# Performance work log

Measured on AMD Instinct MI355X. Metric: run time of the kernel, lower is better.

## Reference

```python
import jax, jax.numpy as jnp
import numpy as np

WINDOW = 13

def setup_inputs() -> dict:
    key = jax.random.key(0)
    ks = jax.random.split(key, 5)
    B, C, D, H, W = 8, 64, 13, 64, 64
    c8 = C // 8
    x = jax.random.normal(ks[0], (B, C, D, H, W), dtype=jnp.float32)
    wq = jax.random.normal(ks[1], (c8, C), dtype=jnp.float32) * 0.1
    wk = jax.random.normal(ks[2], (c8, C), dtype=jnp.float32) * 0.1
    wv = jax.random.normal(ks[3], (C, C), dtype=jnp.float32) * 0.1
    bq = jnp.zeros((c8,), jnp.float32)
    bk = jnp.zeros((c8,), jnp.float32)
    bv = jnp.zeros((C,), jnp.float32)
    return {"x": x, "wq": wq, "bq": bq, "wk": wk, "bk": bk, "wv": wv, "bv": bv}

def reference(x, wq, bq, wk, bk, wv, bv):
    B, C, D, H, W = x.shape
    N = D * H * W
    nb = N // WINDOW  # N chosen divisible by WINDOW
    xf = x.reshape(B, C, N)
    # 1x1 Conv3d == per-voxel channel matmul
    q = jnp.einsum('oc,bcn->bon', wq, xf) + bq[None, :, None]
    k = jnp.einsum('oc,bcn->bon', wk, xf) + bk[None, :, None]
    v = jnp.einsum('oc,bcn->bon', wv, xf) + bv[None, :, None]
    # split flattened spatial dim into independent windows of size 13
    qb = q.reshape(B, -1, nb, WINDOW)
    kb = k.reshape(B, -1, nb, WINDOW)
    vb = v.reshape(B, C, nb, WINDOW)
    # scores[b,n,i,j] = sum_c q[b,c,n,i] * k[b,c,n,j]  (no scaling, as in source)
    scores = jnp.einsum('bcni,bcnj->bnij', qb, kb)
    att = jax.nn.softmax(scores, axis=-1)
    # out[b,c,n,i] = sum_j v[b,c,n,j] * att[b,n,i,j]  (v @ att^T per window)
    out = jnp.einsum('bcnj,bnij->bcni', vb, att)
    return out.reshape(B, C, D, H, W)
```

## Files before the change

kernel.cpp:

```cpp
#include <hip/hip_runtime.h>

#define WINDOW 13
#define NTOT   53248
#define WPB    4
#define VT     52
#define VS     64
#define XS     72
#define QKTS   24

typedef float  floatx4 __attribute__((ext_vector_type(4)));
typedef _Float16 f16x8 __attribute__((ext_vector_type(8)));
typedef __fp16   fp16x2 __attribute__((ext_vector_type(2)));

__device__ __forceinline__ unsigned int pkh2(float a, float b) {
    union { fp16x2 h; unsigned int u; } c;
    c.h = __builtin_amdgcn_cvt_pkrtz(a, b);
    return c.u;
}
__device__ __forceinline__ unsigned short cvt1(float a) {
    union { _Float16 h; unsigned short u; } c;
    c.h = (_Float16)a;
    return c.u;
}

__global__ __launch_bounds__(256)
void prep_kernel(const float* __restrict__ wq, const float* __restrict__ bq,
                 const float* __restrict__ wk, const float* __restrict__ bk,
                 const float* __restrict__ wv, const float* __restrict__ bv,
                 unsigned short* __restrict__ ws)
{
    const int f = blockIdx.x * 256 + threadIdx.x;
    if (f < 640) {
        const int r = f >> 3, cw = (f & 7) * 8;
        const float* src = (r < 8)  ? (wq + r * 64 + cw)
                         : (r < 16) ? (wk + (r - 8) * 64 + cw)
                                    : (wv + (r - 16) * 64 + cw);
        const float4 w0 = *(const float4*)src;
        const float4 w1 = *(const float4*)(src + 4);
        uint4 pk;
        pk.x = pkh2(w0.x, w0.y); pk.y = pkh2(w0.z, w0.w);
        pk.z = pkh2(w1.x, w1.y); pk.w = pkh2(w1.z, w1.w);
        *(uint4*)(ws + r * 64 + cw) = pk;
    } else if (f < 720) {
        const int t = f - 640;
        const float bb = (t < 8) ? bq[t] : (t < 16) ? bk[t - 8] : bv[t - 16];
        ((float*)(ws + 5120))[t] = bb;
    }
}

__global__ __launch_bounds__(512, 8)
void attn_win13_kernel(const float* __restrict__ x,
                       const unsigned short* __restrict__ ws,
                       float* __restrict__ out)
{
    __shared__ __align__(16) unsigned short xT[VS * XS];
    __shared__ __align__(16) unsigned short wbf[80 * XS];
    __shared__ float ball[80];
    __shared__ __align__(16) unsigned short vpad[64 * XS];
    __shared__ __align__(16) unsigned short qkT[VS * QKTS];
    unsigned short* const attb = (unsigned short*)wbf;

    const int tid = threadIdx.x;
    const int b   = blockIdx.y;
    const int v0  = blockIdx.x * VT;
    const size_t total = (size_t)512 * NTOT;

    {
        const int vq = tid >> 5, cp = tid & 31;
        const int c = cp * 2, vx = vq * 4;
        size_t i0 = (size_t)(b * 64 + c) * NTOT + v0 + vx;
        size_t i1 = i0 + NTOT;
        if (i0 > total - 4) i0 = total - 4;
        if (i1 > total - 4) i1 = total - 4;
        const float4 x0 = *(const float4*)(x + i0);
        const float4 x1 = *(const float4*)(x + i1);
        *(unsigned int*)(&xT[(vx + 0) * XS + c]) = pkh2(x0.x, x1.x);
        *(unsigned int*)(&xT[(vx + 1) * XS + c]) = pkh2(x0.y, x1.y);
        *(unsigned int*)(&xT[(vx + 2) * XS + c]) = pkh2(x0.z, x1.z);
        *(unsigned int*)(&xT[(vx + 3) * XS + c]) = pkh2(x0.w, x1.w);
    }
    {
        int f = tid;
#pragma unroll
        for (int it = 0; it < 2; ++it, f += 512) {
            if (f < 640) {
                const int r = f >> 3, cw = (f & 7) * 8;
                const uint4 pk = *(const uint4*)(ws + r * 64 + cw);
                *(uint4*)(&wbf[r * XS + cw]) = pk;
            }
        }
    }
    if (tid < 80) ball[tid] = ((const float*)(ws + 5120))[tid];
    if (tid < 256) {
        const int r = tid >> 2, w = tid & 3;
        const int base = r * XS + w * 16;
        vpad[base + 13] = 0;
        *(unsigned int*)(&vpad[base + 14]) = 0u;
    }
    __syncthreads();

    {
        const int wid  = tid >> 6;
        const int lane = tid & 63;
        const int col  = lane & 15;
        const int g    = lane >> 4;
        for (int t = wid; t < 20; t += 8) {
            const int mt = t >> 2, nt = t & 3;
            const f16x8 xa0 = *(const f16x8*)(&xT [(nt * 16 + col) * XS + g * 8]);
            const f16x8 wa0 = *(const f16x8*)(&wbf[(mt * 16 + col) * XS + g * 8]);
            const f16x8 xa1 = *(const f16x8*)(&xT [(nt * 16 + col) * XS + 32 + g * 8]);
            const f16x8 wa1 = *(const f16x8*)(&wbf[(mt * 16 + col) * XS + 32 + g * 8]);
            floatx4 acc = {0.f, 0.f, 0.f, 0.f};
            acc = __builtin_amdgcn_mfma_f32_16x16x32_f16(xa0, wa0, acc, 0, 0, 0);
            acc = __builtin_amdgcn_mfma_f32_16x16x32_f16(xa1, wa1, acc, 0, 0, 0);
            const int vox = nt * 16 + g * 4;
            if (mt == 0) {
                const float qkb = ball[col];
#pragma unroll
                for (int r = 0; r < 4; ++r)
                    qkT[(vox + r) * QKTS + col] = cvt1(acc[r] + qkb);
            } else {
                const int c_out = (mt - 1) * 16 + col;
                const float vb = ball[16 + c_out];
                int w = vox / 13, j = vox - w * 13;
#pragma unroll
                for (int r = 0; r < 4; ++r) {
                    if (w < WPB) vpad[c_out * XS + w * 16 + j] = cvt1(acc[r] + vb);
                    if (++j == 13) { j = 0; ++w; }
                }
            }
        }
    }
    __syncthreads();

    if (tid < 256) {
        const int wid  = tid >> 6;
        const int lane = tid & 63;
        const int col  = lane & 15;
        const int g    = lane >> 4;
        const f16x8 z = {};
        const f16x8 af = (g < 2) ? *(const f16x8*)(&qkT[(wid * 13 + col) * QKTS + g * 8]) : z;
        const f16x8 bf = (g == 0) ? *(const f16x8*)(&qkT[(wid * 13 + col) * QKTS + 8]) : z;
        floatx4 acc = {0.f, 0.f, 0.f, 0.f};
        acc = __builtin_amdgcn_mfma_f32_16x16x32_f16(af, bf, acc, 0, 0, 0);
#pragma unroll
        for (int r = 0; r < 4; ++r) {
            const float s = (col < 13) ? acc[r] : -1e30f;
            float m = s;
            m = fmaxf(m, __shfl_xor(m, 1));
            m = fmaxf(m, __shfl_xor(m, 2));
            m = fmaxf(m, __shfl_xor(m, 4));
            m = fmaxf(m, __shfl_xor(m, 8));
            const float e = __expf(s - m);
            float sum = e;
            sum += __shfl_xor(sum, 1);
            sum += __shfl_xor(sum, 2);
            sum += __shfl_xor(sum, 4);
            sum += __shfl_xor(sum, 8);
            attb[wid * 256 + (g * 4 + r) * 16 + col] = cvt1(e / sum);
        }
    }
    __syncthreads();

    {
        const int wid  = tid >> 6;
        const int lane = tid & 63;
        const int col  = lane & 15;
        const int g    = lane >> 4;
        const int gA   = g & 1;
        const int w    = wid >> 1;
        const f16x8 z = {};
        const f16x8 bfrag = (g < 2) ? *(const f16x8*)(&attb[w * 256 + col * 16 + g * 8]) : z;
        const size_t obase = (size_t)(b * 64) * NTOT + v0 + w * 13 + col;
#pragma unroll
        for (int q = 0; q < 2; ++q) {
            const int ct = (wid & 1) * 2 + q;
            const f16x8 afrag = *(const f16x8*)(&vpad[(ct * 16 + col) * XS + w * 16 + gA * 8]);
            floatx4 acc = {0.f, 0.f, 0.f, 0.f};
            acc = __builtin_amdgcn_mfma_f32_16x16x32_f16(afrag, bfrag, acc, 0, 0, 0);
            if (col < 13) {
                float* op = out + obase + (size_t)(ct * 16 + g * 4) * NTOT;
                op[0]                = acc[0];
                op[(size_t)NTOT]     = acc[1];
                op[(size_t)2 * NTOT] = acc[2];
                op[(size_t)3 * NTOT] = acc[3];
            }
        }
    }
}

extern "C" void kernel_launch(void* const* d_in, const int* in_sizes, int n_in,
                              void* d_out, int out_size, void* d_ws, size_t ws_size,
                              hipStream_t stream) {
    const float* x  = (const float*)d_in[0];
    const float* wq = (const float*)d_in[1];
    const float* bq = (const float*)d_in[2];
    const float* wk = (const float*)d_in[3];
    const float* bk = (const float*)d_in[4];
    const float* wv = (const float*)d_in[5];
    const float* bv = (const float*)d_in[6];
    float* out = (float*)d_out;
    unsigned short* ws = (unsigned short*)d_ws;

    prep_kernel<<<dim3(3), dim3(256), 0, stream>>>(wq, bq, wk, bk, wv, bv, ws);

    dim3 grid(NTOT / VT, 8);
    dim3 block(512);
    attn_win13_kernel<<<grid, block, 0, stream>>>(x, ws, out);
}
```

Before: 246.4 us.

## Double windows per block to eight and restructure load/compute work split

```diff
diff --git a/kernel.cpp b/kernel.cpp
--- a/kernel.cpp
+++ b/kernel.cpp
@@ -2,11 +2,12 @@
 
 #define WINDOW 13
 #define NTOT   53248
-#define WPB    4
-#define VT     52
-#define VS     64
+#define WPB    8
+#define VT     104
+#define VS     112
 #define XS     72
 #define QKTS   24
+#define VPS    132
 
 typedef float  floatx4 __attribute__((ext_vector_type(4)));
 typedef _Float16 f16x8 __attribute__((ext_vector_type(8)));
@@ -48,7 +49,7 @@
     }
 }
 
-__global__ __launch_bounds__(512, 8)
+__global__ __launch_bounds__(512, 6)
 void attn_win13_kernel(const float* __restrict__ x,
                        const unsigned short* __restrict__ ws,
                        float* __restrict__ out)
@@ -56,7 +57,7 @@
     __shared__ __align__(16) unsigned short xT[VS * XS];
     __shared__ __align__(16) unsigned short wbf[80 * XS];
     __shared__ float ball[80];
-    __shared__ __align__(16) unsigned short vpad[64 * XS];
+    __shared__ __align__(16) unsigned short vpad[64 * VPS];
     __shared__ __align__(16) unsigned short qkT[VS * QKTS];
     unsigned short* const attb = (unsigned short*)wbf;
 
@@ -65,24 +66,30 @@
     const int v0  = blockIdx.x * VT;
     const size_t total = (size_t)512 * NTOT;
 
-    {
-        const int vq = tid >> 5, cp = tid & 31;
-        const int c = cp * 2, vx = vq * 4;
-        size_t i0 = (size_t)(b * 64 + c) * NTOT + v0 + vx;
-        size_t i1 = i0 + NTOT;
-        if (i0 > total - 4) i0 = total - 4;
-        if (i1 > total - 4) i1 = total - 4;
-        const float4 x0 = *(const float4*)(x + i0);
-        const float4 x1 = *(const float4*)(x + i1);
-        *(unsigned int*)(&xT[(vx + 0) * XS + c]) = pkh2(x0.x, x1.x);
-        *(unsigned int*)(&xT[(vx + 1) * XS + c]) = pkh2(x0.y, x1.y);
-        *(unsigned int*)(&xT[(vx + 2) * XS + c]) = pkh2(x0.z, x1.z);
-        *(unsigned int*)(&xT[(vx + 3) * XS + c]) = pkh2(x0.w, x1.w);
-    }
-    {
-        int f = tid;
-#pragma unroll
-        for (int it = 0; it < 2; ++it, f += 512) {
+    if (tid < 224) {
+        const int vq = tid >> 3, cg8 = tid & 7;
+        const int c0 = cg8 * 8, vx = vq * 4;
+        float xv[4][8];
+#pragma unroll
+        for (int i = 0; i < 8; ++i) {
+            size_t idx = (size_t)(b * 64 + c0 + i) * NTOT + v0 + vx;
+            if (idx > total - 4) idx = total - 4;
+            const float4 t = *(const float4*)(x + idx);
+            xv[0][i] = t.x; xv[1][i] = t.y; xv[2][i] = t.z; xv[3][i] = t.w;
+        }
+#pragma unroll
+        for (int r = 0; r < 4; ++r) {
+            uint4 pk;
+            pk.x = pkh2(xv[r][0], xv[r][1]);
+            pk.y = pkh2(xv[r][2], xv[r][3]);
+            pk.z = pkh2(xv[r][4], xv[r][5]);
+            pk.w = pkh2(xv[r][6], xv[r][7]);
+            *(uint4*)(&xT[(vx + r) * XS + c0]) = pk;
+        }
+    } else if (tid >= 256) {
+        int f = tid - 256;
+#pragma unroll
+        for (int it = 0; it < 3; ++it, f += 256) {
             if (f < 640) {
                 const int r = f >> 3, cw = (f & 7) * 8;
                 const uint4 pk = *(const uint4*)(ws + r * 64 + cw);
@@ -90,10 +97,13 @@
             }
         }
     }
-    if (tid < 80) ball[tid] = ((const float*)(ws + 5120))[tid];
-    if (tid < 256) {
-        const int r = tid >> 2, w = tid & 3;
-        const int base = r * XS + w * 16;
+    if (tid >= 432) {
+        const int t2 = tid - 432;
+        ball[t2] = ((const float*)(ws + 5120))[t2];
+    }
+    {
+        const int r = tid >> 3, w = tid & 7;
+        const int base = r * VPS + w * 16;
         vpad[base + 13] = 0;
         *(unsigned int*)(&vpad[base + 14]) = 0u;
     }
@@ -104,8 +114,8 @@
         const int lane = tid & 63;
         const int col  = lane & 15;
         const int g    = lane >> 4;
-        for (int t = wid; t < 20; t += 8) {
-            const int mt = t >> 2, nt = t & 3;
+        for (int t = wid; t < 35; t += 8) {
+            const int mt = t / 7, nt = t % 7;
             const f16x8 xa0 = *(const f16x8*)(&xT [(nt * 16 + col) * XS + g * 8]);
             const f16x8 wa0 = *(const f16x8*)(&wbf[(mt * 16 + col) * XS + g * 8]);
             const f16x8 xa1 = *(const f16x8*)(&xT [(nt * 16 + col) * XS + 32 + g * 8]);
@@ -125,7 +135,7 @@
                 int w = vox / 13, j = vox - w * 13;
 #pragma unroll
                 for (int r = 0; r < 4; ++r) {
-                    if (w < WPB) vpad[c_out * XS + w * 16 + j] = cvt1(acc[r] + vb);
+                    if (w < WPB) vpad[c_out * VPS + w * 16 + j] = cvt1(acc[r] + vb);
                     if (++j == 13) { j = 0; ++w; }
                 }
             }
@@ -133,14 +143,14 @@
     }
     __syncthreads();
 
-    if (tid < 256) {
-        const int wid  = tid >> 6;
+    {
+        const int w    = tid >> 6;
         const int lane = tid & 63;
         const int col  = lane & 15;
         const int g    = lane >> 4;
         const f16x8 z = {};
-        const f16x8 af = (g < 2) ? *(const f16x8*)(&qkT[(wid * 13 + col) * QKTS + g * 8]) : z;
-        const f16x8 bf = (g == 0) ? *(const f16x8*)(&qkT[(wid * 13 + col) * QKTS + 8]) : z;
+        const f16x8 af = (g < 2) ? *(const f16x8*)(&qkT[(w * 13 + col) * QKTS + g * 8]) : z;
+        const f16x8 bf = (g == 0) ? *(const f16x8*)(&qkT[(w * 13 + col) * QKTS + 8]) : z;
         floatx4 acc = {0.f, 0.f, 0.f, 0.f};
         acc = __builtin_amdgcn_mfma_f32_16x16x32_f16(af, bf, acc, 0, 0, 0);
 #pragma unroll
@@ -157,25 +167,23 @@
             sum += __shfl_xor(sum, 2);
             sum += __shfl_xor(sum, 4);
             sum += __shfl_xor(sum, 8);
-            attb[wid * 256 + (g * 4 + r) * 16 + col] = cvt1(e / sum);
+            attb[w * 256 + (g * 4 + r) * 16 + col] = cvt1(e / sum);
         }
     }
     __syncthreads();
 
     {
-        const int wid  = tid >> 6;
+        const int w    = tid >> 6;
         const int lane = tid & 63;
         const int col  = lane & 15;
         const int g    = lane >> 4;
         const int gA   = g & 1;
-        const int w    = wid >> 1;
         const f16x8 z = {};
         const f16x8 bfrag = (g < 2) ? *(const f16x8*)(&attb[w * 256 + col * 16 + g * 8]) : z;
         const size_t obase = (size_t)(b * 64) * NTOT + v0 + w * 13 + col;
 #pragma unroll
-        for (int q = 0; q < 2; ++q) {
-            const int ct = (wid & 1) * 2 + q;
-            const f16x8 afrag = *(const f16x8*)(&vpad[(ct * 16 + col) * XS + w * 16 + gA * 8]);
+        for (int ct = 0; ct < 4; ++ct) {
+            const f16x8 afrag = *(const f16x8*)(&vpad[(ct * 16 + col) * VPS + w * 16 + gA * 8]);
             floatx4 acc = {0.f, 0.f, 0.f, 0.f};
             acc = __builtin_amdgcn_mfma_f32_16x16x32_f16(afrag, bfrag, acc, 0, 0, 0);
             if (col < 13) {
```

Result: faster. 231.1 us (-6.2%).
